# Optimization experiments

Measured on AMD Instinct MI355X. Metric: run time of the kernel, lower is better.

The kernel has to match this reference:

```python
import jax, jax.numpy as jnp
import numpy as np

B, N, K, D, H = 32, 4096, 8, 256, 512
ITERS = 3
LN_EPS = 1e-5  # torch LayerNorm default; self.eps is unused in forward


def _ln(x, g, b):
    m = jnp.mean(x, axis=-1, keepdims=True)
    v = jnp.mean(jnp.square(x - m), axis=-1, keepdims=True)
    return (x - m) * jax.lax.rsqrt(v + LN_EPS) * g + b


def setup_inputs() -> dict:
    key = jax.random.key(0)
    ks = jax.random.split(key, 16)
    s = 0.02
    return {
        "inputs": jax.random.normal(ks[0], (B, N, D), jnp.float32),
        "slots_init": jax.random.normal(ks[1], (B, K, D), jnp.float32),
        "ln_in_g": jnp.ones((D,), jnp.float32), "ln_in_b": jnp.zeros((D,), jnp.float32),
        "ln_s_g": jnp.ones((D,), jnp.float32), "ln_s_b": jnp.zeros((D,), jnp.float32),
        "ln_ff_g": jnp.ones((D,), jnp.float32), "ln_ff_b": jnp.zeros((D,), jnp.float32),
        "Wk": s * jax.random.normal(ks[2], (D, D), jnp.float32), "bk": jnp.zeros((D,), jnp.float32),
        "Wq": s * jax.random.normal(ks[3], (D, D), jnp.float32), "bq": jnp.zeros((D,), jnp.float32),
        "Wv": s * jax.random.normal(ks[4], (D, D), jnp.float32), "bv": jnp.zeros((D,), jnp.float32),
        "W_ih": s * jax.random.normal(ks[5], (3 * D, D), jnp.float32),
        "b_ih": jnp.zeros((3 * D,), jnp.float32),
        "W_hh": s * jax.random.normal(ks[6], (3 * D, D), jnp.float32),
        "b_hh": jnp.zeros((3 * D,), jnp.float32),
        "W1": s * jax.random.normal(ks[7], (H, D), jnp.float32), "b1": jnp.zeros((H,), jnp.float32),
        "W2": s * jax.random.normal(ks[8], (D, H), jnp.float32), "b2": jnp.zeros((D,), jnp.float32),
    }


def _gru_cell(x, h, W_ih, b_ih, W_hh, b_hh):
    # PyTorch GRUCell: gates in order r, z, n
    gi = x @ W_ih.T + b_ih  # [*, 3D]
    gh = h @ W_hh.T + b_hh
    ir, iz, inn = jnp.split(gi, 3, axis=-1)
    hr, hz, hn = jnp.split(gh, 3, axis=-1)
    r = jax.nn.sigmoid(ir + hr)
    z = jax.nn.sigmoid(iz + hz)
    n = jnp.tanh(inn + r * hn)
    return (1.0 - z) * n + z * h


def reference(inputs, slots_init, ln_in_g, ln_in_b, ln_s_g, ln_s_b, ln_ff_g, ln_ff_b,
              Wk, bk, Wq, bq, Wv, bv, W_ih, b_ih, W_hh, b_hh, W1, b1, W2, b2):
    d = inputs.shape[-1]
    x = _ln(inputs, ln_in_g, ln_in_b)  # [B,N,D]
    # k, v depend only on x; hoisted out of the loop (same math as source)
    k = x @ Wk.T + bk                  # project_inputs
    v = x @ Wv.T + bv                  # project_v
    scale = 1.0 / jnp.sqrt(jnp.asarray(d, inputs.dtype))
    slots = slots_init
    for _ in range(ITERS):
        slots_prev = slots
        q = _ln(slots, ln_s_g, ln_s_b) @ Wq.T + bq          # [B,K,D]
        attn_logits = jnp.einsum('bkd,bnd->bkn', q, k) * scale
        # competitive softmax over the SLOT axis (dim=1), not keys
        attn = jax.nn.softmax(attn_logits, axis=1)          # [B,K,N]
        updates = jnp.einsum('bkn,bnd->bkd', attn, v)
        slots = _gru_cell(updates, slots_prev, W_ih, b_ih, W_hh, b_hh)
        hdd = jax.nn.relu(_ln(slots, ln_ff_g, ln_ff_b) @ W1.T + b1)
        slots = slots + hdd @ W2.T + b2
    return slots
```

## Files before the change

### kernel.cpp

```cpp
#include <hip/hip_runtime.h>
#include <hip/hip_bf16.h>
#include <cstddef>
#include <cstdint>

#define BB 32
#define NN 4096
#define KK 8
#define DD 256
#define HH 512
#define LN_EPS 1e-5f
#define SCALE 0.0625f
#define NCHUNK 32

__device__ __forceinline__ float wave_sum(float v) {
#pragma unroll
  for (int off = 32; off >= 1; off >>= 1) v += __shfl_xor(v, off);
  return v;
}

__device__ __forceinline__ float sigmoidf_(float x) { return 1.0f / (1.0f + __expf(-x)); }

__device__ __forceinline__ uint pk2bf(float x, float y) {
  __hip_bfloat16 hx = __float2bfloat16(x), hy = __float2bfloat16(y);
  return (uint)*(ushort*)&hx | ((uint)*(ushort*)&hy << 16);
}

#define OFF_G   0
#define OFF_W1  393216
#define OFF_W2  524288
#define OFF_WV  655360
#define OFF_WQ  720896
#define OFF_WK  786432
#define WB_ELEMS 851968

#define G_PRE (BB * KK)
#define G_W2B (512 * 11)
#define G_SETUP (G_PRE + G_W2B + 1)

__device__ __forceinline__ float dotp4(uint2 w, float4 s) {
  return __uint_as_float(w.x << 16) * s.x + __uint_as_float(w.x & 0xffff0000u) * s.y +
         __uint_as_float(w.y << 16) * s.z + __uint_as_float(w.y & 0xffff0000u) * s.w;
}

template <int OUT, int KL>
__device__ __forceinline__ float gemv_p(const ushort* __restrict__ wt, int j, int kb,
                                        const float* __restrict__ src) {
  const uint2* p = (const uint2*)(wt + ((size_t)(kb >> 2) * OUT + j) * 4);
  float a = 0.0f;
#pragma unroll 16
  for (int e = 0; e < KL / 4; ++e) {
    uint2 w = p[(size_t)e * OUT];
    float4 s = *(const float4*)(src + kb + e * 4);
    a += dotp4(w, s);
  }
  return a;
}

__global__ __launch_bounds__(256) void k_setup(
    const float* __restrict__ Wih, const float* __restrict__ Whh,
    const float* __restrict__ W1, const float* __restrict__ W2,
    const float* __restrict__ Wv, const float* __restrict__ Wq,
    const float* __restrict__ Wk, ushort* __restrict__ wb,
    const float* __restrict__ slots, const float* __restrict__ gs, const float* __restrict__ bs,
    const float* __restrict__ bq, const float* __restrict__ bk,
    const float* __restrict__ gi, const float* __restrict__ bi,
    const float* __restrict__ bv, float* __restrict__ bvw,
    float* __restrict__ qk, float* __restrict__ qb) {
  int blk = blockIdx.x;
  if (blk < G_PRE) {
    int row = blk;
    int t = threadIdx.x;
    int wid = t >> 6, lane = t & 63;
    __shared__ float lns[DD];
    __shared__ float qs[DD];
    __shared__ float rb[8];
    float sv = slots[(size_t)row * DD + t];
    float s = wave_sum(sv);
    float s2 = wave_sum(sv * sv);
    if (lane == 0) { rb[wid] = s; rb[4 + wid] = s2; }
    __syncthreads();
    float tot = rb[0] + rb[1] + rb[2] + rb[3];
    float tot2 = rb[4] + rb[5] + rb[6] + rb[7];
    float m = tot * (1.0f / DD);
    float var = tot2 * (1.0f / DD) - m * m;
    float rs = rsqrtf(var + LN_EPS);
    lns[t] = (sv - m) * rs * gs[t] + bs[t];
    __syncthreads();
    float acc = 0.0f;
    const float4* wr = (const float4*)(Wq + (size_t)t * DD);
#pragma unroll 4
    for (int e4 = 0; e4 < DD / 4; ++e4) {
      float4 w = wr[e4];
      float4 l = ((const float4*)lns)[e4];
      acc += w.x * l.x + w.y * l.y + w.z * l.z + w.w * l.w;
    }
    qs[t] = acc + bq[t];
    __syncthreads();
    float a2 = 0.0f;
    for (int d = 0; d < DD; ++d) a2 = fmaf(qs[d], Wk[(size_t)d * DD + t], a2);
    float a2S = SCALE * a2;
    qk[(size_t)row * DD + t] = a2S * gi[t];
    float pb = wave_sum(qs[t] * bk[t]);
    float pb2 = wave_sum(a2S * bi[t]);
    __syncthreads();
    if (lane == 0) { rb[wid] = pb; rb[4 + wid] = pb2; }
    __syncthreads();
    if (t == 0) qb[row] = SCALE * (rb[0] + rb[1] + rb[2] + rb[3]) + rb[4] + rb[5] + rb[6] + rb[7];
  } else if (blk < G_PRE + G_W2B) {
    int q2 = blk - G_PRE;
    int m = q2 >> 9;
    int idx = (q2 & 511) * 256 + threadIdx.x;
    const int sizes[11] = {65536, 65536, 65536, 65536, 65536, 65536, 131072, 131072, 65536, 65536, 65536};
    const int offs[11] = {OFF_G, OFF_G + 65536, OFF_G + 131072, OFF_G + 196608, OFF_G + 262144,
                          OFF_G + 327680, OFF_W1, OFF_W2, OFF_WV, OFF_WQ, OFF_WK};
    if (idx >= sizes[m]) return;
    int K = (m == 7) ? 512 : 256;
    int OUT = (m == 6) ? 512 : 256;
    int k = idx % K, j = idx / K;
    float v;
    switch (m) {
      case 0: case 1: case 2: v = Wih[((size_t)(m * 256 + j)) * 256 + k]; break;
      case 3: case 4: case 5: v = Whh[((size_t)((m - 3) * 256 + j)) * 256 + k]; break;
      case 6: v = W1[(size_t)j * 256 + k]; break;
      case 7: v = W2[(size_t)j * 512 + k]; break;
      case 8: v = Wv[(size_t)j * 256 + k] * gi[k]; break;
      case 9: v = Wq[(size_t)j * 256 + k]; break;
      default: v = Wk[(size_t)k * 256 + j]; break;
    }
    __hip_bfloat16 h = __float2bfloat16(v);
    wb[(size_t)offs[m] + (size_t)(k >> 2) * OUT * 4 + j * 4 + (k & 3)] = *(ushort*)&h;
  } else {
    int t = threadIdx.x;
    float a = bv[t];
    const float4* wr = (const float4*)(Wv + (size_t)t * DD);
    const float4* bb = (const float4*)bi;
#pragma unroll 4
    for (int e4 = 0; e4 < DD / 4; ++e4) {
      float4 w = wr[e4];
      float4 x = bb[e4];
      a += w.x * x.x + w.y * x.y + w.z * x.z + w.w * x.w;
    }
    bvw[t] = a;
  }
}

template <int DO_LN>
__global__ __launch_bounds__(256, 4) void k_attn_t(const ushort* __restrict__ xb_in,
                                                   ushort* __restrict__ xb_out,
                                                   const float* __restrict__ inp,
                                                   const float* __restrict__ qk,
                                                   const float* __restrict__ qb,
                                                   float* __restrict__ uxp,
                                                   float* __restrict__ sap) {
  typedef __attribute__((ext_vector_type(8))) short short8;
  typedef __attribute__((ext_vector_type(4))) float f32x4;
  union V16 { uint4 u; short8 s; ushort us[8]; };

  __shared__ __align__(16) ushort q_l[16 * 256];
  __shared__ __align__(16) ushort xtile[2][32 * 256];

  int t = threadIdx.x, wid = t >> 6, lane = t & 63;
  int bI = blockIdx.x >> 5, c = blockIdx.x & 31;
  int lm = lane & 15, g = lane >> 4;
  char* qB = (char*)q_l;

  {
    const float* qkb = qk + (size_t)bI * (KK * DD);
    int p = t >> 3, e7 = t & 7;
#pragma unroll 1
    for (int s = 0; s < 8; ++s) {
      float qv = qkb[s * 256 + t];
      __hip_bfloat16 hb = __float2bfloat16(qv);
      float lo = qv - __bfloat162float(hb);
      __hip_bfloat16 lb = __float2bfloat16(lo);
      *(ushort*)(qB + s * 512 + (((p + s) & 31) << 4) + e7 * 2) = *(ushort*)&hb;
      *(ushort*)(qB + (s + 8) * 512 + (((p + s + 8) & 31) << 4) + e7 * 2) = *(ushort*)&lb;
    }
  }
  float qbv = qb[bI * 8 + (lane & 7)];

  f32x4 avacc[4];
#pragma unroll
  for (int i = 0; i < 4; ++i) avacc[i] = (f32x4){0.0f, 0.0f, 0.0f, 0.0f};
  float stot = 0.0f;

  if (!DO_LN) {
    const ushort* s0 = xb_in + ((size_t)bI * NN + c * 128) * DD;
#pragma unroll
    for (int i = 0; i < 4; ++i) {
      __builtin_amdgcn_global_load_lds(
          (__attribute__((address_space(1))) void*)(s0 + i * 2048 + wid * 512 + lane * 8),
          (__attribute__((address_space(3))) void*)(xtile[0] + i * 2048 + wid * 512), 16, 0, 0);
    }
  }

#pragma unroll 1
  for (int tt = 0; tt < 4; ++tt) {
    char* xwB = (char*)xtile[tt & 1];
    int row0 = c * 128 + tt * 32;

    if (DO_LN) {
      __syncthreads();
      int q8 = t & 7, rr = t >> 3;
      const float* rp = inp + ((size_t)bI * NN + row0 + rr) * DD + q8 * 4;
      float4 cur[8];
#pragma unroll
      for (int i = 0; i < 8; ++i) cur[i] = *(const float4*)(rp + i * 32);
      float s1 = 0.0f, s2 = 0.0f;
#pragma unroll
      for (int i = 0; i < 8; ++i) {
        s1 += cur[i].x + cur[i].y + cur[i].z + cur[i].w;
        s2 += cur[i].x * cur[i].x + cur[i].y * cur[i].y + cur[i].z * cur[i].z + cur[i].w * cur[i].w;
      }
      s1 += __shfl_xor(s1, 1); s2 += __shfl_xor(s2, 1);
      s1 += __shfl_xor(s1, 2); s2 += __shfl_xor(s2, 2);
      s1 += __shfl_xor(s1, 4); s2 += __shfl_xor(s2, 4);
      float m = s1 * (1.0f / DD);
      float var = s2 * (1.0f / DD) - m * m;
      float rs = rsqrtf(var + LN_EPS);
      int pb = q8 >> 1, hb8 = (q8 & 1) * 8;
#pragma unroll
      for (int i = 0; i < 8; ++i) {
        uint2 wv;
        wv.x = pk2bf((cur[i].x - m) * rs, (cur[i].y - m) * rs);
        wv.y = pk2bf((cur[i].z - m) * rs, (cur[i].w - m) * rs);
        *(uint2*)(xwB + ((4 * i + pb) << 9) + ((t >> 3) << 4) + hb8) = wv;
      }
      __syncthreads();
      ushort* xbt = xb_out + ((size_t)bI * NN + row0) * DD;
#pragma unroll
      for (int i = 0; i < 4; ++i)
        *(uint4*)((char*)xbt + i * 4096 + t * 16) = *(const uint4*)(xwB + i * 4096 + t * 16);
    } else {
      asm volatile("s_waitcnt vmcnt(0) lgkmcnt(0)" ::: "memory");
      __builtin_amdgcn_sched_barrier(0);
      __builtin_amdgcn_s_barrier();
      __builtin_amdgcn_sched_barrier(0);
      if (tt < 3) {
        const ushort* sn = xb_in + ((size_t)bI * NN + c * 128 + (tt + 1) * 32) * DD;
        ushort* db = xtile[(tt + 1) & 1];
#pragma unroll
        for (int i = 0; i < 4; ++i) {
          __builtin_amdgcn_global_load_lds(
              (__attribute__((address_space(1))) void*)(sn + i * 2048 + wid * 512 + lane * 8),
              (__attribute__((address_space(3))) void*)(db + i * 2048 + wid * 512), 16, 0, 0);
        }
      }
    }

    int rA = lm, rB = lm + 16;
    f32x4 ac0 = {}, ac1 = {};
#pragma unroll
    for (int kk = 0; kk < 8; ++kk) {
      V16 qf, x0, x1;
      int ch = kk * 4 + g;
      qf.u = *(const uint4*)(qB + (lm << 9) + (((ch + lm) & 31) << 4));
      x0.u = *(const uint4*)(xwB + (ch << 9) + (rA << 4));
      x1.u = *(const uint4*)(xwB + (ch << 9) + (rB << 4));
      ac0 = __builtin_amdgcn_mfma_f32_16x16x32_bf16(x0.s, qf.s, ac0, 0, 0, 0);
      ac1 = __builtin_amdgcn_mfma_f32_16x16x32_bf16(x1.s, qf.s, ac1, 0, 0, 0);
    }

    float a0[4], a1[4];
    {
      float lv0[4], lv1[4], mx0[4], mx1[4], ss0[4], ss1[4];
#pragma unroll
      for (int r = 0; r < 4; ++r) {
        lv0[r] = ac0[r] + __shfl_xor(ac0[r], 8) + qbv;
        lv1[r] = ac1[r] + __shfl_xor(ac1[r], 8) + qbv;
        mx0[r] = lv0[r]; mx1[r] = lv1[r];
      }
#pragma unroll
      for (int off = 1; off <= 4; off <<= 1) {
#pragma unroll
        for (int r = 0; r < 4; ++r) {
          mx0[r] = fmaxf(mx0[r], __shfl_xor(mx0[r], off));
          mx1[r] = fmaxf(mx1[r], __shfl_xor(mx1[r], off));
        }
      }
#pragma unroll
      for (int r = 0; r < 4; ++r) {
        a0[r] = __expf(lv0[r] - mx0[r]);
        a1[r] = __expf(lv1[r] - mx1[r]);
        ss0[r] = a0[r]; ss1[r] = a1[r];
      }
#pragma unroll
      for (int off = 1; off <= 4; off <<= 1) {
#pragma unroll
        for (int r = 0; r < 4; ++r) {
          ss0[r] += __shfl_xor(ss0[r], off);
          ss1[r] += __shfl_xor(ss1[r], off);
        }
      }
#pragma unroll
      for (int r = 0; r < 4; ++r) {
        a0[r] *= __frcp_rn(ss0[r]);
        a1[r] *= __frcp_rn(ss1[r]);
      }
    }
    float sacc = 0.0f;
#pragma unroll
    for (int r = 0; r < 4; ++r) sacc += a0[r] + a1[r];
    sacc += __shfl_xor(sacc, 16);
    sacc += __shfl_xor(sacc, 32);
    stot += sacc;

    bool lop = (lane & 8) != 0;
    V16 au;
    {
      float t8[8];
#pragma unroll
      for (int e = 0; e < 8; ++e) {
        float av = (e < 4) ? a0[e] : a1[e - 4];
        if (lop) {
          __hip_bfloat16 hb = __float2bfloat16(av);
          av = av - __bfloat162float(hb);
        }
        t8[e] = av;
      }
      au.u = make_uint4(pk2bf(t8[0], t8[1]), pk2bf(t8[2], t8[3]),
                        pk2bf(t8[4], t8[5]), pk2bf(t8[6], t8[7]));
    }

#pragma unroll
    for (int cc = 0; cc < 4; ++cc) {
      int dc = 4 * wid + cc;
      int d = dc * 16 + lm, dch = d >> 3, d7b = (d & 7) * 2;
      int r0 = 4 * g, r2 = 16 + 4 * g;
      const char* pl = xwB + (dch << 9) + d7b;
      V16 bu;
      bu.u.x = (uint)*(const ushort*)(pl + ((r0 + 0) << 4)) |
               ((uint)*(const ushort*)(pl + ((r0 + 1) << 4)) << 16);
      bu.u.y = (uint)*(const ushort*)(pl + ((r0 + 2) << 4)) |
               ((uint)*(const ushort*)(pl + ((r0 + 3) << 4)) << 16);
      bu.u.z = (uint)*(const ushort*)(pl + ((r2 + 0) << 4)) |
               ((uint)*(const ushort*)(pl + ((r2 + 1) << 4)) << 16);
      bu.u.w = (uint)*(const ushort*)(pl + ((r2 + 2) << 4)) |
               ((uint)*(const ushort*)(pl + ((r2 + 3) << 4)) << 16);
      avacc[cc] = __builtin_amdgcn_mfma_f32_16x16x32_bf16(au.s, bu.s, avacc[cc], 0, 0, 0);
    }
  }

  size_t obase = ((size_t)(bI * NCHUNK + c)) * (KK * DD);
#pragma unroll
  for (int cc = 0; cc < 4; ++cc) {
#pragma unroll
    for (int r = 0; r < 4; ++r) {
      float v = avacc[cc][r];
      float o = v + __shfl_xor(v, 32);
      if (lane < 32) uxp[obase + (g * 4 + r) * 256 + (4 * wid + cc) * 16 + lm] = o;
    }
  }
  if (wid == 0 && lane < 8) sap[((size_t)(bI * NCHUNK + c)) * KK + lane] = stot;
}

__global__ __launch_bounds__(1024) void k_fused(const float* __restrict__ slots_in,
                                                const float* __restrict__ uxp,
                                                const float* __restrict__ sap,
                                                const ushort* __restrict__ wb,
                                                const float* __restrict__ bv,
                                                const float* __restrict__ bih, const float* __restrict__ bhh,
                                                const float* __restrict__ gff, const float* __restrict__ bff,
                                                const float* __restrict__ b1, const float* __restrict__ b2,
                                                const float* __restrict__ gs, const float* __restrict__ bs,
                                                const float* __restrict__ bq, const float* __restrict__ bk,
                                                const float* __restrict__ gi, const float* __restrict__ bi,
                                                float* __restrict__ dst,
                                                float* __restrict__ qk_out,
                                                float* __restrict__ qb_out,
                                                int last) {
  const ushort* WG = wb + OFF_G;
  const ushort* W1p = wb + OFF_W1;
  const ushort* W2p = wb + OFF_W2;
  const ushort* WVp = wb + OFF_WV;
  const ushort* WQp = wb + OFF_WQ;
  const ushort* WKp = wb + OFF_WK;

  __shared__ float ux_s[DD], h_s[DD], upd_s[DD], hn_s[DD], ln_s[DD];
  __shared__ float g_s[6][DD];
  __shared__ float hdd_s[HH];
  __shared__ float tmp4_s[4][DD];
  __shared__ float red_s[16];
  __shared__ float sA_s;
  float* tmpH = &tmp4_s[0][0];

  int t = threadIdx.x, d = t & 255, qr = t >> 8;
  int wid = t >> 6, lane = t & 63;
  int r = blockIdx.x, b = r >> 3, k = r & 7;

  {
    const float* p = uxp + (((size_t)(b * NCHUNK + qr * 8)) * KK + k) * DD + d;
    float s = 0.0f;
#pragma unroll
    for (int i = 0; i < 8; ++i) s += p[(size_t)i * KK * DD];
    tmp4_s[qr][d] = s;
  }
  if (t < 256) h_s[t] = slots_in[(size_t)r * DD + t];
  if (t >= 960) {
    int c = t - 960;
    float v = (c < NCHUNK) ? sap[((size_t)(b * NCHUNK + c)) * KK + k] : 0.0f;
    v = wave_sum(v);
    if (lane == 0) sA_s = v;
  }
  __syncthreads();
  if (t < 256) ux_s[t] = tmp4_s[0][t] + tmp4_s[1][t] + tmp4_s[2][t] + tmp4_s[3][t];
  __syncthreads();

  tmp4_s[qr][d] = gemv_p<256, 64>(WVp, d, qr * 64, ux_s);
  __syncthreads();
  if (t < 256) upd_s[t] = tmp4_s[0][t] + tmp4_s[1][t] + tmp4_s[2][t] + tmp4_s[3][t] + bv[t] * sA_s;
  __syncthreads();

  {
    int g = qr;
    const float* src = (g < 3) ? upd_s : h_s;
    float a = gemv_p<256, 256>(WG + (size_t)g * 65536, d, 0, src);
    g_s[g][d] = a + ((g < 3) ? bih[g * 256 + d] : bhh[d]);
    if (t < 512) {
      int g2 = 4 + (t >> 8), j2 = t & 255;
      float a2 = gemv_p<256, 256>(WG + (size_t)g2 * 65536, j2, 0, h_s);
      g_s[g2][j2] = a2 + bhh[(g2 - 3) * 256 + j2];
    }
  }
  __syncthreads();
  if (t < 256) {
    float rr = sigmoidf_(g_s[0][t] + g_s[3][t]);
    float zz = sigmoidf_(g_s[1][t] + g_s[4][t]);
    float nn = tanhf(g_s[2][t] + rr * g_s[5][t]);
    hn_s[t] = (1.0f - zz) * nn + zz * h_s[t];
  }
  __syncthreads();

  if (t < 256) {
    float v = hn_s[t];
    float sm = wave_sum(v), sq = wave_sum(v * v);
    if (lane == 0) { red_s[wid] = sm; red_s[8 + wid] = sq; }
  }
  __syncthreads();
  if (t < 256) {
    float v = hn_s[t];
    float tot = red_s[0] + red_s[1] + red_s[2] + red_s[3];
    float tot2 = red_s[8] + red_s[9] + red_s[10] + red_s[11];
    float m = tot * (1.0f / DD);
    float var = tot2 * (1.0f / DD) - m * m;
    float rs = rsqrtf(var + LN_EPS);
    ln_s[t] = (v - m) * rs * gff[t] + bff[t];
  }
  __syncthreads();

  {
    int o = t & 511, kh = t >> 9;
    tmpH[kh * 512 + o] = gemv_p<512, 128>(W1p, o, kh * 128, ln_s);
  }
  __syncthreads();
  if (t < 512) hdd_s[t] = fmaxf(tmpH[t] + tmpH[512 + t] + b1[t], 0.0f);
  __syncthreads();

  tmp4_s[qr][d] = gemv_p<256, 128>(W2p, d, qr * 128, hdd_s);
  __syncthreads();
  if (t < 256) {
    float o = hn_s[t] + tmp4_s[0][t] + tmp4_s[1][t] + tmp4_s[2][t] + tmp4_s[3][t] + b2[t];
    dst[(size_t)r * DD + t] = o;
    ux_s[t] = o;
  }
  __syncthreads();

  if (!last) {
    if (t < 256) {
      float v = ux_s[t];
      float sm = wave_sum(v), sq = wave_sum(v * v);
      if (lane == 0) { red_s[wid] = sm; red_s[8 + wid] = sq; }
    }
    __syncthreads();
    if (t < 256) {
      float v = ux_s[t];
      float tot = red_s[0] + red_s[1] + red_s[2] + red_s[3];
      float tot2 = red_s[8] + red_s[9] + red_s[10] + red_s[11];
      float m = tot * (1.0f / DD);
      float var = tot2 * (1.0f / DD) - m * m;
      float rs = rsqrtf(var + LN_EPS);
      ln_s[t] = (v - m) * rs * gs[t] + bs[t];
    }
    __syncthreads();
    tmp4_s[qr][d] = gemv_p<256, 64>(WQp, d, qr * 64, ln_s);
    __syncthreads();
    if (t < 256) {
      float qv = tmp4_s[0][t] + tmp4_s[1][t] + tmp4_s[2][t] + tmp4_s[3][t] + bq[t];
      upd_s[t] = qv;
      float sb = wave_sum(qv * bk[t]);
      if (lane == 0) red_s[wid] = sb;
    }
    __syncthreads();
    {
      float a = gemv_p<256, 64>(WKp, d, qr * 64, upd_s);
      tmp4_s[qr][d] = a;
    }
    __syncthreads();
    if (t < 256) {
      float qkv = SCALE * (tmp4_s[0][t] + tmp4_s[1][t] + tmp4_s[2][t] + tmp4_s[3][t]);
      qk_out[(size_t)r * DD + t] = qkv * gi[t];
      float pb2 = wave_sum(qkv * bi[t]);
      if (lane == 0) red_s[8 + wid] = pb2;
    }
    __syncthreads();
    if (t == 0) qb_out[r] = SCALE * (red_s[0] + red_s[1] + red_s[2] + red_s[3]) +
                            red_s[8] + red_s[9] + red_s[10] + red_s[11];
  }
}

extern "C" void kernel_launch(void* const* d_in, const int* in_sizes, int n_in,
                              void* d_out, int out_size, void* d_ws, size_t ws_size,
                              hipStream_t stream) {
  const float* inputs = (const float*)d_in[0];
  const float* slots_init = (const float*)d_in[1];
  const float* ln_in_g = (const float*)d_in[2];
  const float* ln_in_b = (const float*)d_in[3];
  const float* ln_s_g = (const float*)d_in[4];
  const float* ln_s_b = (const float*)d_in[5];
  const float* ln_ff_g = (const float*)d_in[6];
  const float* ln_ff_b = (const float*)d_in[7];
  const float* Wk = (const float*)d_in[8];
  const float* bk = (const float*)d_in[9];
  const float* Wq = (const float*)d_in[10];
  const float* bq = (const float*)d_in[11];
  const float* Wv = (const float*)d_in[12];
  const float* bv = (const float*)d_in[13];
  const float* Wih = (const float*)d_in[14];
  const float* bih = (const float*)d_in[15];
  const float* Whh = (const float*)d_in[16];
  const float* bhh = (const float*)d_in[17];
  const float* W1 = (const float*)d_in[18];
  const float* b1 = (const float*)d_in[19];
  const float* W2 = (const float*)d_in[20];
  const float* b2 = (const float*)d_in[21];
  float* outp = (float*)d_out;

  char* w = (char*)d_ws;
  ushort* xb = (ushort*)w;       w += (size_t)BB * NN * DD * 2;
  float* qk = (float*)w;         w += (size_t)BB * KK * DD * 4;
  float* qb = (float*)w;         w += (size_t)BB * KK * 4;
  float* uxp = (float*)w;        w += (size_t)BB * NCHUNK * KK * DD * 4;
  float* sap = (float*)w;        w += (size_t)BB * NCHUNK * KK * 4;
  float* slots_ws = (float*)w;   w += (size_t)BB * KK * DD * 4;
  ushort* wb = (ushort*)w;       w += (size_t)WB_ELEMS * 2;
  float* bvw = (float*)w;        w += (size_t)DD * 4;

  k_setup<<<G_SETUP, 256, 0, stream>>>(Wih, Whh, W1, W2, Wv, Wq, Wk, wb,
                                       slots_init, ln_s_g, ln_s_b, bq, bk,
                                       ln_in_g, ln_in_b, bv, bvw, qk, qb);

  for (int it = 0; it < 3; ++it) {
    if (it == 0)
      k_attn_t<1><<<BB * NCHUNK, 256, 0, stream>>>(nullptr, xb, inputs, qk, qb, uxp, sap);
    else
      k_attn_t<0><<<BB * NCHUNK, 256, 0, stream>>>(xb, nullptr, nullptr, qk, qb, uxp, sap);
    const float* sin = (it == 0) ? slots_init : slots_ws;
    float* dst = (it == 2) ? outp : slots_ws;
    k_fused<<<BB * KK, 1024, 0, stream>>>(sin, uxp, sap, wb,
                                          bvw, bih, bhh, ln_ff_g, ln_ff_b, b1, b2,
                                          ln_s_g, ln_s_b, bq, bk, ln_in_g, ln_in_b,
                                          dst, qk, qb, (it == 2) ? 1 : 0);
  }
}
```

Baseline: 231.6 us.

## Merge two attention chunks per 512-thread block sharing the q tile

The attention kernel now runs 512-thread blocks where each half (4 waves) processes its own 128-row chunk, with the two halves sharing one q tile in LDS. Each tile slot is now owned by one half instead of double-buffering, so the global-to-LDS prefetch of the next x tile is dropped and loads are issued synchronously before compute. This halves the q-tile setup work per chunk and splits the hi/lo bf16 conversion across halves, at the cost of losing load/compute overlap within a block and adding block-wide barriers that couple the two halves.

New measurement: 279.3 us. 20.6% more time.

```diff
diff --git a/kernel.cpp b/kernel.cpp
--- a/kernel.cpp
+++ b/kernel.cpp
@@ -145,7 +145,7 @@
 }
 
 template <int DO_LN>
-__global__ __launch_bounds__(256, 4) void k_attn_t(const ushort* __restrict__ xb_in,
+__global__ __launch_bounds__(512, 8) void k_attn_t(const ushort* __restrict__ xb_in,
                                                    ushort* __restrict__ xb_out,
                                                    const float* __restrict__ inp,
                                                    const float* __restrict__ qk,
@@ -160,21 +160,31 @@
   __shared__ __align__(16) ushort xtile[2][32 * 256];
 
   int t = threadIdx.x, wid = t >> 6, lane = t & 63;
-  int bI = blockIdx.x >> 5, c = blockIdx.x & 31;
+  int h = wid >> 2, w4 = wid & 3, th = t & 255;
+  int bI = blockIdx.x >> 4, c = ((blockIdx.x & 15) << 1) + h;
   int lm = lane & 15, g = lane >> 4;
   char* qB = (char*)q_l;
+  ushort* xw = xtile[h];
+  char* xwB = (char*)xw;
 
   {
     const float* qkb = qk + (size_t)bI * (KK * DD);
-    int p = t >> 3, e7 = t & 7;
+    int p = th >> 3, e7 = th & 7;
+    bool lohalf = t >= 256;
 #pragma unroll 1
     for (int s = 0; s < 8; ++s) {
-      float qv = qkb[s * 256 + t];
+      float qv = qkb[s * 256 + th];
       __hip_bfloat16 hb = __float2bfloat16(qv);
-      float lo = qv - __bfloat162float(hb);
-      __hip_bfloat16 lb = __float2bfloat16(lo);
-      *(ushort*)(qB + s * 512 + (((p + s) & 31) << 4) + e7 * 2) = *(ushort*)&hb;
-      *(ushort*)(qB + (s + 8) * 512 + (((p + s + 8) & 31) << 4) + e7 * 2) = *(ushort*)&lb;
+      ushort st;
+      if (!lohalf) {
+        st = *(ushort*)&hb;
+      } else {
+        float lo = qv - __bfloat162float(hb);
+        __hip_bfloat16 lb = __float2bfloat16(lo);
+        st = *(ushort*)&lb;
+      }
+      int sr = lohalf ? (s + 8) : s;
+      *(ushort*)(qB + sr * 512 + (((p + sr) & 31) << 4) + e7 * 2) = st;
     }
   }
   float qbv = qb[bI * 8 + (lane & 7)];
@@ -184,24 +194,13 @@
   for (int i = 0; i < 4; ++i) avacc[i] = (f32x4){0.0f, 0.0f, 0.0f, 0.0f};
   float stot = 0.0f;
 
-  if (!DO_LN) {
-    const ushort* s0 = xb_in + ((size_t)bI * NN + c * 128) * DD;
-#pragma unroll
-    for (int i = 0; i < 4; ++i) {
-      __builtin_amdgcn_global_load_lds(
-          (__attribute__((address_space(1))) void*)(s0 + i * 2048 + wid * 512 + lane * 8),
-          (__attribute__((address_space(3))) void*)(xtile[0] + i * 2048 + wid * 512), 16, 0, 0);
-    }
-  }
-
 #pragma unroll 1
   for (int tt = 0; tt < 4; ++tt) {
-    char* xwB = (char*)xtile[tt & 1];
     int row0 = c * 128 + tt * 32;
+    __syncthreads();
 
     if (DO_LN) {
-      __syncthreads();
-      int q8 = t & 7, rr = t >> 3;
+      int q8 = th & 7, rr = th >> 3;
       const float* rp = inp + ((size_t)bI * NN + row0 + rr) * DD + q8 * 4;
       float4 cur[8];
 #pragma unroll
@@ -224,28 +223,24 @@
         uint2 wv;
         wv.x = pk2bf((cur[i].x - m) * rs, (cur[i].y - m) * rs);
         wv.y = pk2bf((cur[i].z - m) * rs, (cur[i].w - m) * rs);
-        *(uint2*)(xwB + ((4 * i + pb) << 9) + ((t >> 3) << 4) + hb8) = wv;
+        *(uint2*)(xwB + ((4 * i + pb) << 9) + (rr << 4) + hb8) = wv;
       }
       __syncthreads();
       ushort* xbt = xb_out + ((size_t)bI * NN + row0) * DD;
 #pragma unroll
       for (int i = 0; i < 4; ++i)
-        *(uint4*)((char*)xbt + i * 4096 + t * 16) = *(const uint4*)(xwB + i * 4096 + t * 16);
+        *(uint4*)((char*)xbt + i * 4096 + th * 16) = *(const uint4*)(xwB + i * 4096 + th * 16);
     } else {
+      const ushort* srcb = xb_in + ((size_t)bI * NN + row0) * DD;
+#pragma unroll
+      for (int i = 0; i < 4; ++i) {
+        __builtin_amdgcn_global_load_lds(
+            (__attribute__((address_space(1))) void*)(srcb + i * 2048 + w4 * 512 + lane * 8),
+            (__attribute__((address_space(3))) void*)(xw + i * 2048 + w4 * 512), 16, 0, 0);
+      }
       asm volatile("s_waitcnt vmcnt(0) lgkmcnt(0)" ::: "memory");
       __builtin_amdgcn_sched_barrier(0);
-      __builtin_amdgcn_s_barrier();
-      __builtin_amdgcn_sched_barrier(0);
-      if (tt < 3) {
-        const ushort* sn = xb_in + ((size_t)bI * NN + c * 128 + (tt + 1) * 32) * DD;
-        ushort* db = xtile[(tt + 1) & 1];
-#pragma unroll
-        for (int i = 0; i < 4; ++i) {
-          __builtin_amdgcn_global_load_lds(
-              (__attribute__((address_space(1))) void*)(sn + i * 2048 + wid * 512 + lane * 8),
-              (__attribute__((address_space(3))) void*)(db + i * 2048 + wid * 512), 16, 0, 0);
-        }
-      }
+      __syncthreads();
     }
 
     int rA = lm, rB = lm + 16;
@@ -324,7 +319,7 @@
 
 #pragma unroll
     for (int cc = 0; cc < 4; ++cc) {
-      int dc = 4 * wid + cc;
+      int dc = 4 * w4 + cc;
       int d = dc * 16 + lm, dch = d >> 3, d7b = (d & 7) * 2;
       int r0 = 4 * g, r2 = 16 + 4 * g;
       const char* pl = xwB + (dch << 9) + d7b;
@@ -348,10 +343,10 @@
     for (int r = 0; r < 4; ++r) {
       float v = avacc[cc][r];
       float o = v + __shfl_xor(v, 32);
-      if (lane < 32) uxp[obase + (g * 4 + r) * 256 + (4 * wid + cc) * 16 + lm] = o;
-    }
-  }
-  if (wid == 0 && lane < 8) sap[((size_t)(bI * NCHUNK + c)) * KK + lane] = stot;
+      if (lane < 32) uxp[obase + (g * 4 + r) * 256 + (4 * w4 + cc) * 16 + lm] = o;
+    }
+  }
+  if (w4 == 0 && lane < 8) sap[((size_t)(bI * NCHUNK + c)) * KK + lane] = stot;
 }
 
 __global__ __launch_bounds__(1024) void k_fused(const float* __restrict__ slots_in,
@@ -551,9 +546,9 @@
 
   for (int it = 0; it < 3; ++it) {
     if (it == 0)
-      k_attn_t<1><<<BB * NCHUNK, 256, 0, stream>>>(nullptr, xb, inputs, qk, qb, uxp, sap);
+      k_attn_t<1><<<BB * 16, 512, 0, stream>>>(nullptr, xb, inputs, qk, qb, uxp, sap);
     else
-      k_attn_t<0><<<BB * NCHUNK, 256, 0, stream>>>(xb, nullptr, nullptr, qk, qb, uxp, sap);
+      k_attn_t<0><<<BB * 16, 512, 0, stream>>>(xb, nullptr, nullptr, qk, qb, uxp, sap);
     const float* sin = (it == 0) ? slots_init : slots_ws;
     float* dst = (it == 2) ? outp : slots_ws;
     k_fused<<<BB * KK, 1024, 0, stream>>>(sin, uxp, sap, wb,
```
